# Kernel optimization log

Hardware: AMD Instinct MI355X
Metric: run time of the kernel (lower is better)

Reference implementation:

```python
import jax, jax.numpy as jnp
import numpy as np

B, N, DIM, H = 2, 2048, 1024, 16
D = DIM // H  # head_dim = 64


def setup_inputs() -> dict:
    key = jax.random.key(0)
    k1, k2, k3, k4, k5 = jax.random.split(key, 5)
    x = jax.random.normal(k1, (B, N, DIM), dtype=jnp.float32)
    # nn.Linear weights: [out_features, in_features]; scaled for stable softmax
    qkv_w = jax.random.normal(k2, (3 * DIM, DIM), dtype=jnp.float32) * (DIM ** -0.5)
    qkv_b = jax.random.normal(k3, (3 * DIM,), dtype=jnp.float32) * 0.02
    proj_w = jax.random.normal(k4, (DIM, DIM), dtype=jnp.float32) * (DIM ** -0.5)
    proj_b = jax.random.normal(k5, (DIM,), dtype=jnp.float32) * 0.02
    return {"x": x, "qkv_w": qkv_w, "qkv_b": qkv_b, "proj_w": proj_w, "proj_b": proj_b}


def reference(x, qkv_w, qkv_b, proj_w, proj_b):
    b, n, c = x.shape
    # qkv linear: [B,N,3C] -> [B,N,3,H,D] -> q,k,v each [B,H,N,D]
    qkv = x @ qkv_w.T + qkv_b
    qkv = qkv.reshape(b, n, 3, H, D).transpose(2, 0, 3, 1, 4)
    q, k, v = qkv[0], qkv[1], qkv[2]
    # scaled dot-product attention (no dropout, no mask); qk_norm=False, rope=None
    scale = D ** -0.5
    scores = jnp.einsum("bhqd,bhkd->bhqk", q, k) * scale
    attn = jax.nn.softmax(scores, axis=-1)
    out = jnp.einsum("bhqk,bhkd->bhqd", attn, v)
    # [B,H,N,D] -> [B,N,C]
    out = out.transpose(0, 2, 1, 3).reshape(b, n, c)
    # output projection
    return out @ proj_w.T + proj_b
```

## Files before the change

kernel.cpp:

```cpp
#include <hip/hip_runtime.h>
#include <hip/hip_bf16.h>
#include <math.h>

typedef __attribute__((ext_vector_type(8))) short short8v;
typedef __attribute__((ext_vector_type(4))) float f32x4;
typedef unsigned short ushort_t;

__device__ __forceinline__ ushort_t to_bf16(float v) {
    __hip_bfloat16 h = __float2bfloat16(v);
    return *(ushort_t*)&h;
}

__device__ __forceinline__ unsigned cvt_pk_bf16(float a, float b) {
    unsigned r;
    asm("v_cvt_pk_bf16_f32 %0, %1, %2" : "=v"(r) : "v"(a), "v"(b));
    return r;
}

__device__ __forceinline__ void load_lds_16B(const void* g, void* l) {
    __builtin_amdgcn_global_load_lds(
        (__attribute__((address_space(1))) unsigned int*)(g),
        (__attribute__((address_space(3))) unsigned int*)(l), 16, 0, 0);
}

__global__ __launch_bounds__(256) void convert_kernel(
    const float* __restrict__ x, const float* __restrict__ wq,
    const float* __restrict__ wp, ushort_t* __restrict__ xb,
    ushort_t* __restrict__ wqb, ushort_t* __restrict__ wpb)
{
    int c = blockIdx.x * 256 + threadIdx.x;
    const float* src; ushort_t* dst; int base;
    if (c < 524288)      { src = x;  dst = xb;  base = c; }
    else if (c < 917504) { src = wq; dst = wqb; base = c - 524288; }
    else                 { src = wp; dst = wpb; base = c - 917504; }
    const float4* s4 = (const float4*)src;
    float4 a = s4[2 * (size_t)base], b = s4[2 * (size_t)base + 1];
    float vals[8] = {a.x, a.y, a.z, a.w, b.x, b.y, b.z, b.w};
    short8v o;
#pragma unroll
    for (int j = 0; j < 8; j++) o[j] = (short)to_bf16(vals[j]);
    *(short8v*)(dst + 8 * (size_t)base) = o;
}

template <int MODE, int BM, int BN>
__global__ __launch_bounds__(256) void gemm_bf16_kernel(
    const ushort_t* __restrict__ A, const ushort_t* __restrict__ Bw,
    const float* __restrict__ bias, ushort_t* __restrict__ Qb,
    ushort_t* __restrict__ Kb, ushort_t* __restrict__ Vt,
    float* __restrict__ Cout)
{
    constexpr int MT = BM / 32, NT = BN / 32;
    __shared__ __align__(16) ushort_t As[BM * 32];
    __shared__ __align__(16) ushort_t Bs[BN * 32];
    const int t = threadIdx.x;
    const int w = t >> 6, l = t & 63;
    const int lo = l & 15, hi = l >> 4;
    const int wr = w >> 1, wc = w & 1;
    const int m0 = blockIdx.y * BM, n0 = blockIdx.x * BN;
    const int K = 1024;

    const ushort_t* ga = A + (size_t)(m0 + (t >> 2)) * K + (t & 3) * 8;
    const ushort_t* gb = Bw + (size_t)(n0 + (t >> 2)) * K + (t & 3) * 8;

    f32x4 acc[MT][NT] = {};

    for (int k0 = 0; k0 < 1024; k0 += 32) {
#pragma unroll
        for (int i = 0; i < BM / 64; i++)
            load_lds_16B(ga + (size_t)(i * 64) * K + k0, As + (i * 256 + w * 64) * 8);
#pragma unroll
        for (int i = 0; i < BN / 64; i++)
            load_lds_16B(gb + (size_t)(i * 64) * K + k0, Bs + (i * 256 + w * 64) * 8);
        __syncthreads();

        short8v af[MT], bf[NT];
#pragma unroll
        for (int mt = 0; mt < MT; mt++) {
            int r = wr * (BM / 2) + mt * 16 + lo;
            af[mt] = *(const short8v*)&As[r * 32 + hi * 8];
        }
#pragma unroll
        for (int nt = 0; nt < NT; nt++) {
            int r = wc * (BN / 2) + nt * 16 + lo;
            bf[nt] = *(const short8v*)&Bs[r * 32 + hi * 8];
        }
#pragma unroll
        for (int mt = 0; mt < MT; mt++)
#pragma unroll
            for (int nt = 0; nt < NT; nt++)
                acc[mt][nt] = __builtin_amdgcn_mfma_f32_16x16x32_bf16(
                    af[mt], bf[nt], acc[mt][nt], 0, 0, 0);
        __syncthreads();
    }

#pragma unroll
    for (int mt = 0; mt < MT; mt++) {
#pragma unroll
        for (int nt = 0; nt < NT; nt++) {
            int col = n0 + wc * (BN / 2) + nt * 16 + lo;
            float bv = bias[col];
#pragma unroll
            for (int reg = 0; reg < 4; reg++) {
                int row = m0 + wr * (BM / 2) + mt * 16 + hi * 4 + reg;
                float val = acc[mt][nt][reg] + bv;
                if constexpr (MODE == 0) {
                    int bb = row >> 11, n = row & 2047;
                    int which = col >> 10, rem = col & 1023;
                    int h = rem >> 6, d = rem & 63;
                    int bh = bb * 16 + h;
                    if (which == 0)
                        Qb[((size_t)bh * 2048 + n) * 64 + d] = to_bf16(val * 0.1803368601f);
                    else if (which == 1)
                        Kb[((size_t)bh * 2048 + n) * 64 + d] = to_bf16(val);
                    else
                        Vt[((size_t)bh * 64 + d) * 2048 + n] = to_bf16(val);
                } else {
                    Cout[(size_t)row * 1024 + col] = val;
                }
            }
        }
    }
}

__global__ __launch_bounds__(256) void attn_mfma_kernel(
    const ushort_t* __restrict__ Qg0, const ushort_t* __restrict__ Kg0,
    const ushort_t* __restrict__ Vg0, ushort_t* __restrict__ O)
{
    __shared__ __align__(16) ushort_t Ks[2 * 64 * 64];
    __shared__ __align__(16) ushort_t Vs[2 * 64 * 64];

    const int t = threadIdx.x;
    const int l = t & 63, w = t >> 6;
    const int lo = l & 15, hi = l >> 4;
    const int lin = (blockIdx.x & 7) * 64 + (blockIdx.x >> 3);
    const int bh = lin >> 4;
    const int q0 = (lin & 15) * 128;
    const ushort_t* Qg = Qg0 + (size_t)bh * 2048 * 64;
    const ushort_t* Kg = Kg0 + (size_t)bh * 2048 * 64;
    const ushort_t* Vg = Vg0 + (size_t)bh * 64 * 2048;

    short8v aq[2][2];
#pragma unroll
    for (int qf = 0; qf < 2; qf++) {
        const ushort_t* qrow = Qg + (size_t)(q0 + w * 32 + qf * 16 + lo) * 64;
        aq[qf][0] = *(const short8v*)(qrow + hi * 8);
        aq[qf][1] = *(const short8v*)(qrow + 32 + hi * 8);
    }

    const int srow = t >> 3, sg = t & 7;
    const int sgs = sg ^ (srow & 7);
    const int gv0 = (sg >> 2) * 4 + (sg & 1) * 2;
    const int vo = ((sg >> 1) & 1) * 4;
    const int vswz0 = srow & 7;
    uint4 rk0, rk1, rv0, rv1;

    f32x4 o_acc[2][4] = {};
    float m_i[2] = {-INFINITY, -INFINITY};
    float l_i[2] = {0.0f, 0.0f};

    {
        rk0 = *(const uint4*)(Kg + (size_t)srow * 64 + sg * 8);
        rk1 = *(const uint4*)(Kg + (size_t)(srow + 32) * 64 + sg * 8);
        rv0 = *(const uint4*)(Vg + (size_t)srow * 2048 + sg * 8);
        rv1 = *(const uint4*)(Vg + (size_t)(srow + 32) * 2048 + sg * 8);
        *(uint4*)&Ks[srow * 64 + sgs * 8] = rk0;
        *(uint4*)&Ks[(srow + 32) * 64 + sgs * 8] = rk1;
        uint2 va0 = {rv0.x, rv0.y}, vb0 = {rv0.z, rv0.w};
        uint2 va1 = {rv1.x, rv1.y}, vb1 = {rv1.z, rv1.w};
        *(uint2*)&Vs[srow * 64 + (gv0 ^ vswz0) * 8 + vo] = va0;
        *(uint2*)&Vs[srow * 64 + ((gv0 + 1) ^ vswz0) * 8 + vo] = vb0;
        *(uint2*)&Vs[(srow + 32) * 64 + (gv0 ^ vswz0) * 8 + vo] = va1;
        *(uint2*)&Vs[(srow + 32) * 64 + ((gv0 + 1) ^ vswz0) * 8 + vo] = vb1;
    }
    __syncthreads();

    for (int kt = 0; kt < 32; kt++) {
        const int bufo = (kt & 1) * 4096;
        if (kt < 31) {
            const int k0n = (kt + 1) * 64;
            rk0 = *(const uint4*)(Kg + (size_t)(k0n + srow) * 64 + sg * 8);
            rk1 = *(const uint4*)(Kg + (size_t)(k0n + srow + 32) * 64 + sg * 8);
            rv0 = *(const uint4*)(Vg + (size_t)srow * 2048 + k0n + sg * 8);
            rv1 = *(const uint4*)(Vg + (size_t)(srow + 32) * 2048 + k0n + sg * 8);
        }

        f32x4 s_acc[2][4];
        __builtin_amdgcn_s_setprio(1);
#pragma unroll
        for (int nt = 0; nt < 4; nt++) {
            f32x4 acc0 = {0.f, 0.f, 0.f, 0.f};
            f32x4 acc1 = {0.f, 0.f, 0.f, 0.f};
#pragma unroll
            for (int kk = 0; kk < 2; kk++) {
                int r = nt * 16 + lo;
                int g = (kk * 4 + hi) ^ (r & 7);
                short8v ak = *(const short8v*)&Ks[bufo + r * 64 + g * 8];
                acc0 = __builtin_amdgcn_mfma_f32_16x16x32_bf16(ak, aq[0][kk], acc0, 0, 0, 0);
                acc1 = __builtin_amdgcn_mfma_f32_16x16x32_bf16(ak, aq[1][kk], acc1, 0, 0, 0);
            }
            s_acc[0][nt] = acc0;
            s_acc[1][nt] = acc1;
        }
        __builtin_amdgcn_s_setprio(0);

        short8v pa[2][2];
#pragma unroll
        for (int qf = 0; qf < 2; qf++) {
            float pm = fmaxf(
                fmaxf(fmaxf(fmaxf(s_acc[qf][0][0], s_acc[qf][0][1]),
                            fmaxf(s_acc[qf][0][2], s_acc[qf][0][3])),
                      fmaxf(fmaxf(s_acc[qf][1][0], s_acc[qf][1][1]),
                            fmaxf(s_acc[qf][1][2], s_acc[qf][1][3]))),
                fmaxf(fmaxf(fmaxf(s_acc[qf][2][0], s_acc[qf][2][1]),
                            fmaxf(s_acc[qf][2][2], s_acc[qf][2][3])),
                      fmaxf(fmaxf(s_acc[qf][3][0], s_acc[qf][3][1]),
                            fmaxf(s_acc[qf][3][2], s_acc[qf][3][3]))));
            pm = fmaxf(pm, __shfl_xor(pm, 16));
            pm = fmaxf(pm, __shfl_xor(pm, 32));

            if (__any(pm > m_i[qf] + 11.0f)) {
                float mnew = fmaxf(m_i[qf], pm);
                float al = __builtin_amdgcn_exp2f(m_i[qf] - mnew);
                m_i[qf] = mnew;
                l_i[qf] *= al;
                float a0 = __shfl(al, hi * 4 + 0);
                float a1 = __shfl(al, hi * 4 + 1);
                float a2 = __shfl(al, hi * 4 + 2);
                float a3 = __shfl(al, hi * 4 + 3);
#pragma unroll
                for (int dt = 0; dt < 4; dt++) {
                    o_acc[qf][dt][0] *= a0; o_acc[qf][dt][1] *= a1;
                    o_acc[qf][dt][2] *= a2; o_acc[qf][dt][3] *= a3;
                }
            }

            float ps = 0.0f;
#pragma unroll
            for (int nt = 0; nt < 4; nt++)
#pragma unroll
                for (int reg = 0; reg < 4; reg++) {
                    s_acc[qf][nt][reg] =
                        __builtin_amdgcn_exp2f(s_acc[qf][nt][reg] - m_i[qf]);
                    ps += s_acc[qf][nt][reg];
                }
            ps += __shfl_xor(ps, 16);
            ps += __shfl_xor(ps, 32);
            l_i[qf] += ps;

            int4 w0i = {(int)cvt_pk_bf16(s_acc[qf][0][0], s_acc[qf][0][1]),
                        (int)cvt_pk_bf16(s_acc[qf][0][2], s_acc[qf][0][3]),
                        (int)cvt_pk_bf16(s_acc[qf][1][0], s_acc[qf][1][1]),
                        (int)cvt_pk_bf16(s_acc[qf][1][2], s_acc[qf][1][3])};
            int4 w1i = {(int)cvt_pk_bf16(s_acc[qf][2][0], s_acc[qf][2][1]),
                        (int)cvt_pk_bf16(s_acc[qf][2][2], s_acc[qf][2][3]),
                        (int)cvt_pk_bf16(s_acc[qf][3][0], s_acc[qf][3][1]),
                        (int)cvt_pk_bf16(s_acc[qf][3][2], s_acc[qf][3][3])};
            pa[qf][0] = __builtin_bit_cast(short8v, w0i);
            pa[qf][1] = __builtin_bit_cast(short8v, w1i);
        }

        if (kt < 31) {
            const int nxto = 4096 - bufo;
            *(uint4*)&Ks[nxto + srow * 64 + sgs * 8] = rk0;
            *(uint4*)&Ks[nxto + (srow + 32) * 64 + sgs * 8] = rk1;
            uint2 va0 = {rv0.x, rv0.y}, vb0 = {rv0.z, rv0.w};
            uint2 va1 = {rv1.x, rv1.y}, vb1 = {rv1.z, rv1.w};
            *(uint2*)&Vs[nxto + srow * 64 + (gv0 ^ vswz0) * 8 + vo] = va0;
            *(uint2*)&Vs[nxto + srow * 64 + ((gv0 + 1) ^ vswz0) * 8 + vo] = vb0;
            *(uint2*)&Vs[nxto + (srow + 32) * 64 + (gv0 ^ vswz0) * 8 + vo] = va1;
            *(uint2*)&Vs[nxto + (srow + 32) * 64 + ((gv0 + 1) ^ vswz0) * 8 + vo] = vb1;
        }

        __builtin_amdgcn_s_setprio(1);
#pragma unroll
        for (int dt = 0; dt < 4; dt++) {
            int r = dt * 16 + lo;
            short8v bv0 = *(const short8v*)&Vs[bufo + r * 64 + ((0 + hi) ^ (r & 7)) * 8];
            short8v bv1 = *(const short8v*)&Vs[bufo + r * 64 + ((4 + hi) ^ (r & 7)) * 8];
            o_acc[0][dt] = __builtin_amdgcn_mfma_f32_16x16x32_bf16(pa[0][0], bv0, o_acc[0][dt], 0, 0, 0);
            o_acc[0][dt] = __builtin_amdgcn_mfma_f32_16x16x32_bf16(pa[0][1], bv1, o_acc[0][dt], 0, 0, 0);
            o_acc[1][dt] = __builtin_amdgcn_mfma_f32_16x16x32_bf16(pa[1][0], bv0, o_acc[1][dt], 0, 0, 0);
            o_acc[1][dt] = __builtin_amdgcn_mfma_f32_16x16x32_bf16(pa[1][1], bv1, o_acc[1][dt], 0, 0, 0);
        }
        __builtin_amdgcn_s_setprio(0);
        __syncthreads();
    }

    const int b = bh >> 4, h = bh & 15;
#pragma unroll
    for (int qf = 0; qf < 2; qf++) {
#pragma unroll
        for (int reg = 0; reg < 4; reg++) {
            float lv = __shfl(l_i[qf], hi * 4 + reg);
            float inv = 1.0f / lv;
            int row = q0 + w * 32 + qf * 16 + hi * 4 + reg;
            ushort_t* orow = O + ((size_t)(b * 2048 + row)) * 1024 + h * 64;
#pragma unroll
            for (int dt = 0; dt < 4; dt++)
                orow[dt * 16 + lo] = to_bf16(o_acc[qf][dt][reg] * inv);
        }
    }
}

extern "C" void kernel_launch(void* const* d_in, const int* in_sizes, int n_in,
                              void* d_out, int out_size, void* d_ws, size_t ws_size,
                              hipStream_t stream) {
    const float* x      = (const float*)d_in[0];
    const float* qkv_w  = (const float*)d_in[1];
    const float* qkv_b  = (const float*)d_in[2];
    const float* proj_w = (const float*)d_in[3];
    const float* proj_b = (const float*)d_in[4];
    float* out = (float*)d_out;

    ushort_t* xb  = (ushort_t*)d_ws;
    ushort_t* wqb = xb  + 4194304;
    ushort_t* wpb = wqb + 3145728;
    ushort_t* qb  = wpb + 1048576;
    ushort_t* kb  = qb  + 4194304;
    ushort_t* vt  = kb  + 4194304;
    ushort_t* aob = vt  + 4194304;

    convert_kernel<<<4096, 256, 0, stream>>>(x, qkv_w, proj_w, xb, wqb, wpb);
    gemm_bf16_kernel<0, 128, 128><<<dim3(24, 32), 256, 0, stream>>>(
        xb, wqb, qkv_b, qb, kb, vt, nullptr);
    attn_mfma_kernel<<<512, 256, 0, stream>>>(qb, kb, vt, aob);
    gemm_bf16_kernel<1, 128, 128><<<dim3(8, 32), 256, 0, stream>>>(
        aob, wpb, proj_b, nullptr, nullptr, nullptr, out);
}
```

Baseline: 131.9 us.

## Split attention along the key dimension and merge partials in a combine kernel

Each attention block now handles half of the keys for a 128-query tile, which doubles the grid from 512 to 1024 blocks so the GPU's compute units are better filled. Each half writes a normalized partial output plus its row max and sum. A new combine kernel then merges the two halves with log-sum-exp weights into the head-interleaved layout. The output-projection GEMM also switches to a 64-row tile with twice as many blocks. The costs are an extra kernel launch, extra global traffic for the partial outputs, and extra bf16 rounding of the partials.

```diff
diff --git a/kernel.cpp b/kernel.cpp
--- a/kernel.cpp
+++ b/kernel.cpp
@@ -9,6 +9,11 @@
 __device__ __forceinline__ ushort_t to_bf16(float v) {
     __hip_bfloat16 h = __float2bfloat16(v);
     return *(ushort_t*)&h;
+}
+
+__device__ __forceinline__ float bf2f(ushort_t u) {
+    unsigned x = ((unsigned)u) << 16;
+    return __builtin_bit_cast(float, x);
 }
 
 __device__ __forceinline__ unsigned cvt_pk_bf16(float a, float b) {
@@ -124,7 +129,8 @@
 
 __global__ __launch_bounds__(256) void attn_mfma_kernel(
     const ushort_t* __restrict__ Qg0, const ushort_t* __restrict__ Kg0,
-    const ushort_t* __restrict__ Vg0, ushort_t* __restrict__ O)
+    const ushort_t* __restrict__ Vg0, ushort_t* __restrict__ op0,
+    ushort_t* __restrict__ op1, float* __restrict__ ml)
 {
     __shared__ __align__(16) ushort_t Ks[2 * 64 * 64];
     __shared__ __align__(16) ushort_t Vs[2 * 64 * 64];
@@ -132,12 +138,14 @@
     const int t = threadIdx.x;
     const int l = t & 63, w = t >> 6;
     const int lo = l & 15, hi = l >> 4;
-    const int lin = (blockIdx.x & 7) * 64 + (blockIdx.x >> 3);
-    const int bh = lin >> 4;
-    const int q0 = (lin & 15) * 128;
+    const int lin = (blockIdx.x & 7) * 128 + (blockIdx.x >> 3);
+    const int bh = lin >> 5;
+    const int unit = lin & 31;
+    const int q0 = (unit >> 1) * 128;
+    const int s = unit & 1;
     const ushort_t* Qg = Qg0 + (size_t)bh * 2048 * 64;
-    const ushort_t* Kg = Kg0 + (size_t)bh * 2048 * 64;
-    const ushort_t* Vg = Vg0 + (size_t)bh * 64 * 2048;
+    const ushort_t* Kg = Kg0 + (size_t)bh * 2048 * 64 + (size_t)s * 1024 * 64;
+    const ushort_t* Vg = Vg0 + (size_t)bh * 64 * 2048 + (size_t)s * 1024;
 
     short8v aq[2][2];
 #pragma unroll
@@ -174,9 +182,9 @@
     }
     __syncthreads();
 
-    for (int kt = 0; kt < 32; kt++) {
+    for (int kt = 0; kt < 16; kt++) {
         const int bufo = (kt & 1) * 4096;
-        if (kt < 31) {
+        if (kt < 15) {
             const int k0n = (kt + 1) * 64;
             rk0 = *(const uint4*)(Kg + (size_t)(k0n + srow) * 64 + sg * 8);
             rk1 = *(const uint4*)(Kg + (size_t)(k0n + srow + 32) * 64 + sg * 8);
@@ -259,7 +267,7 @@
             pa[qf][1] = __builtin_bit_cast(short8v, w1i);
         }
 
-        if (kt < 31) {
+        if (kt < 15) {
             const int nxto = 4096 - bufo;
             *(uint4*)&Ks[nxto + srow * 64 + sgs * 8] = rk0;
             *(uint4*)&Ks[nxto + (srow + 32) * 64 + sgs * 8] = rk1;
@@ -286,20 +294,53 @@
         __syncthreads();
     }
 
-    const int b = bh >> 4, h = bh & 15;
+    ushort_t* opart = s ? op1 : op0;
+    const int qbase = q0 + w * 32;
 #pragma unroll
     for (int qf = 0; qf < 2; qf++) {
+        if (hi == 0) {
+            float2 v; v.x = m_i[qf]; v.y = l_i[qf];
+            ((float2*)ml)[(size_t)s * 65536 + bh * 2048 + qbase + qf * 16 + lo] = v;
+        }
 #pragma unroll
         for (int reg = 0; reg < 4; reg++) {
             float lv = __shfl(l_i[qf], hi * 4 + reg);
             float inv = 1.0f / lv;
-            int row = q0 + w * 32 + qf * 16 + hi * 4 + reg;
-            ushort_t* orow = O + ((size_t)(b * 2048 + row)) * 1024 + h * 64;
+            int row = qbase + qf * 16 + hi * 4 + reg;
+            ushort_t* orow = opart + ((size_t)bh * 2048 + row) * 64;
 #pragma unroll
             for (int dt = 0; dt < 4; dt++)
                 orow[dt * 16 + lo] = to_bf16(o_acc[qf][dt][reg] * inv);
         }
     }
+}
+
+__global__ __launch_bounds__(256) void combine_kernel(
+    const ushort_t* __restrict__ op0, const ushort_t* __restrict__ op1,
+    const float* __restrict__ ml, ushort_t* __restrict__ aob)
+{
+    int idx = blockIdx.x * 256 + threadIdx.x;
+    int bhq = idx >> 3, c = idx & 7;
+    const float2* mlp = (const float2*)ml;
+    float2 ml0 = mlp[bhq];
+    float2 ml1 = mlp[65536 + bhq];
+    float mstar = fmaxf(ml0.x, ml1.x);
+    float w0 = __builtin_amdgcn_exp2f(ml0.x - mstar) * ml0.y;
+    float w1 = __builtin_amdgcn_exp2f(ml1.x - mstar) * ml1.y;
+    float inv = 1.0f / (w0 + w1);
+    float b0 = w0 * inv, b1 = w1 * inv;
+    short8v a = *(const short8v*)(op0 + (size_t)bhq * 64 + c * 8);
+    short8v bq = *(const short8v*)(op1 + (size_t)bhq * 64 + c * 8);
+    float r[8];
+#pragma unroll
+    for (int j = 0; j < 8; j++)
+        r[j] = b0 * bf2f((ushort_t)a[j]) + b1 * bf2f((ushort_t)bq[j]);
+    int4 oi = {(int)cvt_pk_bf16(r[0], r[1]), (int)cvt_pk_bf16(r[2], r[3]),
+               (int)cvt_pk_bf16(r[4], r[5]), (int)cvt_pk_bf16(r[6], r[7])};
+    int bh = bhq >> 11, n = bhq & 2047;
+    int b = bh >> 4, h = bh & 15;
+    *(short8v*)(aob + ((size_t)(b * 2048 + n)) * 1024 + h * 64 + c * 8) =
+        __builtin_bit_cast(short8v, oi);
 }
 
 extern "C" void kernel_launch(void* const* d_in, const int* in_sizes, int n_in,
@@ -319,11 +360,15 @@
     ushort_t* kb  = qb  + 4194304;
     ushort_t* vt  = kb  + 4194304;
     ushort_t* aob = vt  + 4194304;
+    ushort_t* op0 = xb;
+    ushort_t* op1 = aob + 4194304;
+    float*    ml  = (float*)(op1 + 4194304);
 
     convert_kernel<<<4096, 256, 0, stream>>>(x, qkv_w, proj_w, xb, wqb, wpb);
     gemm_bf16_kernel<0, 128, 128><<<dim3(24, 32), 256, 0, stream>>>(
         xb, wqb, qkv_b, qb, kb, vt, nullptr);
-    attn_mfma_kernel<<<512, 256, 0, stream>>>(qb, kb, vt, aob);
-    gemm_bf16_kernel<1, 128, 128><<<dim3(8, 32), 256, 0, stream>>>(
+    attn_mfma_kernel<<<1024, 256, 0, stream>>>(qb, kb, vt, op0, op1, ml);
+    combine_kernel<<<2048, 256, 0, stream>>>(op0, op1, ml, aob);
+    gemm_bf16_kernel<1, 64, 128><<<dim3(8, 64), 256, 0, stream>>>(
         aob, wpb, proj_b, nullptr, nullptr, nullptr, out);
 }
```

New measurement: 134.0 us. Within noise of the previous version (+1.6%).

## Software-pipeline attention QK of next tile with softmax/PV of current tile

Applied to the files above, without the earlier changes.

Restructures the attention loop so the QK^T MFMAs for tile T+1 are issued before the softmax and PV of tile T. It uses a triple-buffered V LDS ring and double-buffered K, unrolled by two, so MFMA work can overlap the exp/reduction VALU work. It also changes the output projection GEMM to 64-row tiles with twice as many blocks, to fill more CUs. The cost is extra registers for two score tiles and more LDS, which may lower occupancy.

```diff
diff --git a/kernel.cpp b/kernel.cpp
--- a/kernel.cpp
+++ b/kernel.cpp
@@ -126,8 +126,8 @@
     const ushort_t* __restrict__ Qg0, const ushort_t* __restrict__ Kg0,
     const ushort_t* __restrict__ Vg0, ushort_t* __restrict__ O)
 {
-    __shared__ __align__(16) ushort_t Ks[2 * 64 * 64];
-    __shared__ __align__(16) ushort_t Vs[2 * 64 * 64];
+    __shared__ __align__(16) ushort_t Ks[2 * 4096];
+    __shared__ __align__(16) ushort_t Vs[3 * 4096];
 
     const int t = threadIdx.x;
     const int l = t & 63, w = t >> 6;
@@ -155,66 +155,59 @@
     uint4 rk0, rk1, rv0, rv1;
 
     f32x4 o_acc[2][4] = {};
+    f32x4 sE[2][4], sO[2][4];
     float m_i[2] = {-INFINITY, -INFINITY};
     float l_i[2] = {0.0f, 0.0f};
 
-    {
-        rk0 = *(const uint4*)(Kg + (size_t)srow * 64 + sg * 8);
-        rk1 = *(const uint4*)(Kg + (size_t)(srow + 32) * 64 + sg * 8);
-        rv0 = *(const uint4*)(Vg + (size_t)srow * 2048 + sg * 8);
-        rv1 = *(const uint4*)(Vg + (size_t)(srow + 32) * 2048 + sg * 8);
-        *(uint4*)&Ks[srow * 64 + sgs * 8] = rk0;
-        *(uint4*)&Ks[(srow + 32) * 64 + sgs * 8] = rk1;
+    auto gload = [&](int kt) {
+        const int k0n = kt * 64;
+        rk0 = *(const uint4*)(Kg + (size_t)(k0n + srow) * 64 + sg * 8);
+        rk1 = *(const uint4*)(Kg + (size_t)(k0n + srow + 32) * 64 + sg * 8);
+        rv0 = *(const uint4*)(Vg + (size_t)srow * 2048 + k0n + sg * 8);
+        rv1 = *(const uint4*)(Vg + (size_t)(srow + 32) * 2048 + k0n + sg * 8);
+    };
+    auto stage_write = [&](int kslot, int vslot) {
+        *(uint4*)&Ks[kslot * 4096 + srow * 64 + sgs * 8] = rk0;
+        *(uint4*)&Ks[kslot * 4096 + (srow + 32) * 64 + sgs * 8] = rk1;
         uint2 va0 = {rv0.x, rv0.y}, vb0 = {rv0.z, rv0.w};
         uint2 va1 = {rv1.x, rv1.y}, vb1 = {rv1.z, rv1.w};
-        *(uint2*)&Vs[srow * 64 + (gv0 ^ vswz0) * 8 + vo] = va0;
-        *(uint2*)&Vs[srow * 64 + ((gv0 + 1) ^ vswz0) * 8 + vo] = vb0;
-        *(uint2*)&Vs[(srow + 32) * 64 + (gv0 ^ vswz0) * 8 + vo] = va1;
-        *(uint2*)&Vs[(srow + 32) * 64 + ((gv0 + 1) ^ vswz0) * 8 + vo] = vb1;
-    }
-    __syncthreads();
-
-    for (int kt = 0; kt < 32; kt++) {
-        const int bufo = (kt & 1) * 4096;
-        if (kt < 31) {
-            const int k0n = (kt + 1) * 64;
-            rk0 = *(const uint4*)(Kg + (size_t)(k0n + srow) * 64 + sg * 8);
-            rk1 = *(const uint4*)(Kg + (size_t)(k0n + srow + 32) * 64 + sg * 8);
-            rv0 = *(const uint4*)(Vg + (size_t)srow * 2048 + k0n + sg * 8);
-            rv1 = *(const uint4*)(Vg + (size_t)(srow + 32) * 2048 + k0n + sg * 8);
-        }
-
-        f32x4 s_acc[2][4];
+        *(uint2*)&Vs[vslot * 4096 + srow * 64 + (gv0 ^ vswz0) * 8 + vo] = va0;
+        *(uint2*)&Vs[vslot * 4096 + srow * 64 + ((gv0 + 1) ^ vswz0) * 8 + vo] = vb0;
+        *(uint2*)&Vs[vslot * 4096 + (srow + 32) * 64 + (gv0 ^ vswz0) * 8 + vo] = va1;
+        *(uint2*)&Vs[vslot * 4096 + (srow + 32) * 64 + ((gv0 + 1) ^ vswz0) * 8 + vo] = vb1;
+    };
+    auto qk = [&](f32x4 (&sd)[2][4], int kslot) {
         __builtin_amdgcn_s_setprio(1);
 #pragma unroll
         for (int nt = 0; nt < 4; nt++) {
-            f32x4 acc0 = {0.f, 0.f, 0.f, 0.f};
-            f32x4 acc1 = {0.f, 0.f, 0.f, 0.f};
+            f32x4 a0 = {0.f, 0.f, 0.f, 0.f};
+            f32x4 a1 = {0.f, 0.f, 0.f, 0.f};
 #pragma unroll
             for (int kk = 0; kk < 2; kk++) {
                 int r = nt * 16 + lo;
                 int g = (kk * 4 + hi) ^ (r & 7);
-                short8v ak = *(const short8v*)&Ks[bufo + r * 64 + g * 8];
-                acc0 = __builtin_amdgcn_mfma_f32_16x16x32_bf16(ak, aq[0][kk], acc0, 0, 0, 0);
-                acc1 = __builtin_amdgcn_mfma_f32_16x16x32_bf16(ak, aq[1][kk], acc1, 0, 0, 0);
+                short8v ak = *(const short8v*)&Ks[kslot * 4096 + r * 64 + g * 8];
+                a0 = __builtin_amdgcn_mfma_f32_16x16x32_bf16(ak, aq[0][kk], a0, 0, 0, 0);
+                a1 = __builtin_amdgcn_mfma_f32_16x16x32_bf16(ak, aq[1][kk], a1, 0, 0, 0);
             }
-            s_acc[0][nt] = acc0;
-            s_acc[1][nt] = acc1;
+            sd[0][nt] = a0;
+            sd[1][nt] = a1;
         }
         __builtin_amdgcn_s_setprio(0);
-
+    };
+    auto softmax_pv = [&](f32x4 (&sc)[2][4], int vslot) {
         short8v pa[2][2];
 #pragma unroll
         for (int qf = 0; qf < 2; qf++) {
             float pm = fmaxf(
-                fmaxf(fmaxf(fmaxf(s_acc[qf][0][0], s_acc[qf][0][1]),
-                            fmaxf(s_acc[qf][0][2], s_acc[qf][0][3])),
-                      fmaxf(fmaxf(s_acc[qf][1][0], s_acc[qf][1][1]),
-                            fmaxf(s_acc[qf][1][2], s_acc[qf][1][3]))),
-                fmaxf(fmaxf(fmaxf(s_acc[qf][2][0], s_acc[qf][2][1]),
-                            fmaxf(s_acc[qf][2][2], s_acc[qf][2][3])),
-                      fmaxf(fmaxf(s_acc[qf][3][0], s_acc[qf][3][1]),
-                            fmaxf(s_acc[qf][3][2], s_acc[qf][3][3]))));
+                fmaxf(fmaxf(fmaxf(sc[qf][0][0], sc[qf][0][1]),
+                            fmaxf(sc[qf][0][2], sc[qf][0][3])),
+                      fmaxf(fmaxf(sc[qf][1][0], sc[qf][1][1]),
+                            fmaxf(sc[qf][1][2], sc[qf][1][3]))),
+                fmaxf(fmaxf(fmaxf(sc[qf][2][0], sc[qf][2][1]),
+                            fmaxf(sc[qf][2][2], sc[qf][2][3])),
+                      fmaxf(fmaxf(sc[qf][3][0], sc[qf][3][1]),
+                            fmaxf(sc[qf][3][2], sc[qf][3][3]))));
             pm = fmaxf(pm, __shfl_xor(pm, 16));
             pm = fmaxf(pm, __shfl_xor(pm, 32));
 
@@ -239,51 +232,65 @@
             for (int nt = 0; nt < 4; nt++)
 #pragma unroll
                 for (int reg = 0; reg < 4; reg++) {
-                    s_acc[qf][nt][reg] =
-                        __builtin_amdgcn_exp2f(s_acc[qf][nt][reg] - m_i[qf]);
-                    ps += s_acc[qf][nt][reg];
+                    sc[qf][nt][reg] =
+                        __builtin_amdgcn_exp2f(sc[qf][nt][reg] - m_i[qf]);
+                    ps += sc[qf][nt][reg];
                 }
             ps += __shfl_xor(ps, 16);
             ps += __shfl_xor(ps, 32);
             l_i[qf] += ps;
 
-            int4 w0i = {(int)cvt_pk_bf16(s_acc[qf][0][0], s_acc[qf][0][1]),
-                        (int)cvt_pk_bf16(s_acc[qf][0][2], s_acc[qf][0][3]),
-                        (int)cvt_pk_bf16(s_acc[qf][1][0], s_acc[qf][1][1]),
-                        (int)cvt_pk_bf16(s_acc[qf][1][2], s_acc[qf][1][3])};
-            int4 w1i = {(int)cvt_pk_bf16(s_acc[qf][2][0], s_acc[qf][2][1]),
-                        (int)cvt_pk_bf16(s_acc[qf][2][2], s_acc[qf][2][3]),
-                        (int)cvt_pk_bf16(s_acc[qf][3][0], s_acc[qf][3][1]),
-                        (int)cvt_pk_bf16(s_acc[qf][3][2], s_acc[qf][3][3])};
+            int4 w0i = {(int)cvt_pk_bf16(sc[qf][0][0], sc[qf][0][1]),
+                        (int)cvt_pk_bf16(sc[qf][0][2], sc[qf][0][3]),
+                        (int)cvt_pk_bf16(sc[qf][1][0], sc[qf][1][1]),
+                        (int)cvt_pk_bf16(sc[qf][1][2], sc[qf][1][3])};
+            int4 w1i = {(int)cvt_pk_bf16(sc[qf][2][0], sc[qf][2][1]),
+                        (int)cvt_pk_bf16(sc[qf][2][2], sc[qf][2][3]),
+                        (int)cvt_pk_bf16(sc[qf][3][0], sc[qf][3][1]),
+                        (int)cvt_pk_bf16(sc[qf][3][2], sc[qf][3][3])};
             pa[qf][0] = __builtin_bit_cast(short8v, w0i);
             pa[qf][1] = __builtin_bit_cast(short8v, w1i);
         }
 
-        if (kt < 31) {
-            const int nxto = 4096 - bufo;
-            *(uint4*)&Ks[nxto + srow * 64 + sgs * 8] = rk0;
-            *(uint4*)&Ks[nxto + (srow + 32) * 64 + sgs * 8] = rk1;
-            uint2 va0 = {rv0.x, rv0.y}, vb0 = {rv0.z, rv0.w};
-            uint2 va1 = {rv1.x, rv1.y}, vb1 = {rv1.z, rv1.w};
-            *(uint2*)&Vs[nxto + srow * 64 + (gv0 ^ vswz0) * 8 + vo] = va0;
-            *(uint2*)&Vs[nxto + srow * 64 + ((gv0 + 1) ^ vswz0) * 8 + vo] = vb0;
-            *(uint2*)&Vs[nxto + (srow + 32) * 64 + (gv0 ^ vswz0) * 8 + vo] = va1;
-            *(uint2*)&Vs[nxto + (srow + 32) * 64 + ((gv0 + 1) ^ vswz0) * 8 + vo] = vb1;
-        }
-
         __builtin_amdgcn_s_setprio(1);
 #pragma unroll
         for (int dt = 0; dt < 4; dt++) {
             int r = dt * 16 + lo;
-            short8v bv0 = *(const short8v*)&Vs[bufo + r * 64 + ((0 + hi) ^ (r & 7)) * 8];
-            short8v bv1 = *(const short8v*)&Vs[bufo + r * 64 + ((4 + hi) ^ (r & 7)) * 8];
+            short8v bv0 = *(const short8v*)&Vs[vslot * 4096 + r * 64 + ((0 + hi) ^ (r & 7)) * 8];
+            short8v bv1 = *(const short8v*)&Vs[vslot * 4096 + r * 64 + ((4 + hi) ^ (r & 7)) * 8];
             o_acc[0][dt] = __builtin_amdgcn_mfma_f32_16x16x32_bf16(pa[0][0], bv0, o_acc[0][dt], 0, 0, 0);
             o_acc[0][dt] = __builtin_amdgcn_mfma_f32_16x16x32_bf16(pa[0][1], bv1, o_acc[0][dt], 0, 0, 0);
             o_acc[1][dt] = __builtin_amdgcn_mfma_f32_16x16x32_bf16(pa[1][0], bv0, o_acc[1][dt], 0, 0, 0);
             o_acc[1][dt] = __builtin_amdgcn_mfma_f32_16x16x32_bf16(pa[1][1], bv1, o_acc[1][dt], 0, 0, 0);
         }
         __builtin_amdgcn_s_setprio(0);
+    };
+
+    gload(0);
+    stage_write(0, 0);
+    gload(1);
+    __syncthreads();
+    qk(sE, 0);
+
+    int v0 = 0;
+    for (int ti = 0; ti < 16; ti++) {
+        const int T = 2 * ti;
+        int v1 = v0 + 1; if (v1 == 3) v1 = 0;
+        int v2 = v1 + 1; if (v2 == 3) v2 = 0;
+
+        stage_write(1, v1);
+        if (T + 2 < 32) gload(T + 2);
         __syncthreads();
+        qk(sO, 1);
+        softmax_pv(sE, v0);
+
+        if (T + 2 < 32) stage_write(0, v2);
+        if (T + 3 < 32) gload(T + 3);
+        __syncthreads();
+        if (T + 2 < 32) qk(sE, 0);
+        softmax_pv(sO, v1);
+
+        v0 = v2;
     }
 
     const int b = bh >> 4, h = bh & 15;
@@ -324,6 +331,6 @@
     gemm_bf16_kernel<0, 128, 128><<<dim3(24, 32), 256, 0, stream>>>(
         xb, wqb, qkv_b, qb, kb, vt, nullptr);
     attn_mfma_kernel<<<512, 256, 0, stream>>>(qb, kb, vt, aob);
-    gemm_bf16_kernel<1, 128, 128><<<dim3(8, 32), 256, 0, stream>>>(
+    gemm_bf16_kernel<1, 64, 128><<<dim3(8, 64), 256, 0, stream>>>(
         aob, wpb, proj_b, nullptr, nullptr, nullptr, out);
 }
```

Result: faster. 127.0 us (-3.8%).

## Remap QKV GEMM blocks per XCD, defer softmax row-sum reduction, shrink proj tile

Applied to the files above, without the earlier changes.

The QKV GEMM now runs on a 1D grid whose block index is remapped so that consecutive blocks on each XCD (blockIdx & 7) cover neighbouring output tiles. This aims to improve L2 reuse of A and B tiles. In attention, the cross-lane reduction of the row max now happens only inside the rare rescale branch, and the per-lane partial sums are reduced once at the end instead of every tile, which removes shuffles from the inner loop. The output projection uses 64x128 tiles, giving 512 blocks instead of 256 for better occupancy across CUs, at the cost of less reuse per block.

```diff
diff --git a/kernel.cpp b/kernel.cpp
--- a/kernel.cpp
+++ b/kernel.cpp
@@ -56,7 +56,15 @@
     const int w = t >> 6, l = t & 63;
     const int lo = l & 15, hi = l >> 4;
     const int wr = w >> 1, wc = w & 1;
-    const int m0 = blockIdx.y * BM, n0 = blockIdx.x * BN;
+    int m0, n0;
+    if constexpr (MODE == 0) {
+        int lin = (blockIdx.x & 7) * 96 + (blockIdx.x >> 3);
+        m0 = (lin / 24) * BM;
+        n0 = (lin % 24) * BN;
+    } else {
+        m0 = blockIdx.y * BM;
+        n0 = blockIdx.x * BN;
+    }
     const int K = 1024;
 
     const ushort_t* ga = A + (size_t)(m0 + (t >> 2)) * K + (t & 3) * 8;
@@ -156,7 +164,7 @@
 
     f32x4 o_acc[2][4] = {};
     float m_i[2] = {-INFINITY, -INFINITY};
-    float l_i[2] = {0.0f, 0.0f};
+    float lp[2] = {0.0f, 0.0f};
 
     {
         rk0 = *(const uint4*)(Kg + (size_t)srow * 64 + sg * 8);
@@ -206,7 +214,7 @@
         short8v pa[2][2];
 #pragma unroll
         for (int qf = 0; qf < 2; qf++) {
-            float pm = fmaxf(
+            float lmax = fmaxf(
                 fmaxf(fmaxf(fmaxf(s_acc[qf][0][0], s_acc[qf][0][1]),
                             fmaxf(s_acc[qf][0][2], s_acc[qf][0][3])),
                       fmaxf(fmaxf(s_acc[qf][1][0], s_acc[qf][1][1]),
@@ -215,14 +223,14 @@
                             fmaxf(s_acc[qf][2][2], s_acc[qf][2][3])),
                       fmaxf(fmaxf(s_acc[qf][3][0], s_acc[qf][3][1]),
                             fmaxf(s_acc[qf][3][2], s_acc[qf][3][3]))));
-            pm = fmaxf(pm, __shfl_xor(pm, 16));
-            pm = fmaxf(pm, __shfl_xor(pm, 32));
-
-            if (__any(pm > m_i[qf] + 11.0f)) {
+
+            if (__any(lmax > m_i[qf] + 11.0f)) {
+                float pm = fmaxf(lmax, __shfl_xor(lmax, 16));
+                pm = fmaxf(pm, __shfl_xor(pm, 32));
                 float mnew = fmaxf(m_i[qf], pm);
                 float al = __builtin_amdgcn_exp2f(m_i[qf] - mnew);
                 m_i[qf] = mnew;
-                l_i[qf] *= al;
+                lp[qf] *= al;
                 float a0 = __shfl(al, hi * 4 + 0);
                 float a1 = __shfl(al, hi * 4 + 1);
                 float a2 = __shfl(al, hi * 4 + 2);
@@ -243,9 +251,7 @@
                         __builtin_amdgcn_exp2f(s_acc[qf][nt][reg] - m_i[qf]);
                     ps += s_acc[qf][nt][reg];
                 }
-            ps += __shfl_xor(ps, 16);
-            ps += __shfl_xor(ps, 32);
-            l_i[qf] += ps;
+            lp[qf] += ps;
 
             int4 w0i = {(int)cvt_pk_bf16(s_acc[qf][0][0], s_acc[qf][0][1]),
                         (int)cvt_pk_bf16(s_acc[qf][0][2], s_acc[qf][0][3]),
@@ -289,9 +295,12 @@
     const int b = bh >> 4, h = bh & 15;
 #pragma unroll
     for (int qf = 0; qf < 2; qf++) {
+        float ls = lp[qf];
+        ls += __shfl_xor(ls, 16);
+        ls += __shfl_xor(ls, 32);
 #pragma unroll
         for (int reg = 0; reg < 4; reg++) {
-            float lv = __shfl(l_i[qf], hi * 4 + reg);
+            float lv = __shfl(ls, hi * 4 + reg);
             float inv = 1.0f / lv;
             int row = q0 + w * 32 + qf * 16 + hi * 4 + reg;
             ushort_t* orow = O + ((size_t)(b * 2048 + row)) * 1024 + h * 64;
@@ -321,9 +330,9 @@
     ushort_t* aob = vt  + 4194304;
 
     convert_kernel<<<4096, 256, 0, stream>>>(x, qkv_w, proj_w, xb, wqb, wpb);
-    gemm_bf16_kernel<0, 128, 128><<<dim3(24, 32), 256, 0, stream>>>(
+    gemm_bf16_kernel<0, 128, 128><<<768, 256, 0, stream>>>(
         xb, wqb, qkv_b, qb, kb, vt, nullptr);
     attn_mfma_kernel<<<512, 256, 0, stream>>>(qb, kb, vt, aob);
-    gemm_bf16_kernel<1, 128, 128><<<dim3(8, 32), 256, 0, stream>>>(
+    gemm_bf16_kernel<1, 64, 128><<<dim3(8, 64), 256, 0, stream>>>(
         aob, wpb, proj_b, nullptr, nullptr, nullptr, out);
 }
```

After: 122.8 us. 1.07x faster.
